# Kernel tuning notes

Measured on AMD Instinct MI355X. Metric: run time of the kernel, lower is better.

## Reference

```python
import jax, jax.numpy as jnp
import numpy as np

L = 3          # encoder layers
H, D = 12, 64  # heads, head_dim
DM = H * D     # 768
DF = 3072
WH = WW = 14
S = WH * WW + 1            # 197 tokens incl. cls
ND = (2*WH-1)*(2*WW-1) + 3  # 732 rel-pos entries
EPS = 1e-12


def _make_rel_idx():
    coords = np.stack(np.meshgrid(np.arange(WH), np.arange(WW), indexing='ij'))
    coords = coords.reshape(2, -1)                      # [2, 196]
    rel = (coords[:, :, None] - coords[:, None, :]).transpose(1, 2, 0)  # [196,196,2]
    rel[:, :, 0] += WH - 1
    rel[:, :, 1] += WW - 1
    rel[:, :, 0] *= 2 * WW - 1
    idx = np.zeros((S, S), dtype=np.int32)
    idx[1:, 1:] = rel.sum(-1)
    idx[0, :] = ND - 3
    idx[:, 0] = ND - 2
    idx[0, 0] = ND - 1
    return jnp.asarray(idx.flatten())

REL_IDX = _make_rel_idx()


def _ln(x, g, b):
    m = jnp.mean(x, -1, keepdims=True)
    v = jnp.mean(jnp.square(x - m), -1, keepdims=True)
    return (x - m) * jax.lax.rsqrt(v + EPS) * g + b


def setup_inputs() -> dict:
    key = jax.random.key(0)
    ks = iter(jax.random.split(key, 32))
    p = lambda *s: jax.random.normal(next(ks), s, jnp.float32) * 0.02
    inp = {
        'x': jax.random.normal(next(ks), (64, WH, WW, DM), jnp.float32),
        'cls': p(1, 1, DM),
        'g1': jnp.ones((L, DM)), 'b1': jnp.zeros((L, DM)),
        'Wq': p(L, DM, DM), 'bq': jnp.zeros((L, DM)),
        'Wk': p(L, DM, DM),
        'Wv': p(L, DM, DM), 'bv': jnp.zeros((L, DM)),
        'rel_tbl': p(L, ND, H),
        'Wo': p(L, DM, DM), 'bo': jnp.zeros((L, DM)),
        'lam1': jnp.full((L, DM), 0.1),
        'g2': jnp.ones((L, DM)), 'b2': jnp.zeros((L, DM)),
        'Wi': p(L, DM, DF), 'bi': jnp.zeros((L, DF)),
        'Wmo': p(L, DF, DM), 'bmo': jnp.zeros((L, DM)),
        'lam2': jnp.full((L, DM), 0.1),
    }
    return inp


def reference(x, cls, g1, b1, Wq, bq, Wk, Wv, bv, rel_tbl, Wo, bo, lam1,
              g2, b2, Wi, bi, Wmo, bmo, lam2):
    B = x.shape[0]
    # patchemb: NHWC -> NCHW -> [B, C, HW] -> [B, HW, C], prepend cls token
    t = jnp.transpose(x, (0, 3, 1, 2)).reshape(B, DM, WH * WW)
    t = jnp.transpose(t, (0, 2, 1))
    h = jnp.concatenate([jnp.broadcast_to(cls, (B, 1, DM)), t], axis=1)  # [B,S,DM]

    scale = 1.0 / np.sqrt(D)
    for i in range(L):
        r = h
        hn = _ln(h, g1[i], b1[i])
        q = (hn @ Wq[i] + bq[i]).reshape(B, S, H, D)
        k = (hn @ Wk[i]).reshape(B, S, H, D)
        v = (hn @ Wv[i] + bv[i]).reshape(B, S, H, D)
        scores = jnp.einsum('bqhd,bkhd->bhqk', q, k) * scale   # [B,H,S,S]
        rel = rel_tbl[i][REL_IDX].reshape(S, S, H)             # gather bias table
        scores = scores + jnp.transpose(rel, (2, 0, 1))[None]
        probs = jax.nn.softmax(scores, axis=-1)
        ctx = jnp.einsum('bhqk,bkhd->bqhd', probs, v).reshape(B, S, DM)
        h = r + (ctx @ Wo[i] + bo[i]) * lam1[i]
        r = h
        hn = _ln(h, g2[i], b2[i])
        ff = jax.nn.gelu(hn @ Wi[i] + bi[i], approximate=False) @ Wmo[i] + bmo[i]
        h = r + ff * lam2[i]
    return h  # final encoder output [B, S, DM]
```

## Files before the change

kernel.cpp:

```cpp
#include <hip/hip_runtime.h>

#define DMM 768
#define DFF 3072
#define NH  12
#define HD  64
#define SQ  197
#define BA  64
#define NDD 732
#define MROWS (BA*SQ)
#define MPAD  12672
#define PCOLS 224
#define KS2   72
#define VTS   232
#define QS    2304
#define BIASN (NH*208*208)

typedef unsigned short u16;
typedef __bf16 bf16x8 __attribute__((ext_vector_type(8)));
typedef float  f32x4  __attribute__((ext_vector_type(4)));
typedef unsigned short us8 __attribute__((ext_vector_type(8)));

__device__ __forceinline__ u16 f2b(float f) {
    unsigned v; __builtin_memcpy(&v, &f, 4);
    unsigned r = v + 0x7FFFu + ((v >> 16) & 1u);
    return (u16)(r >> 16);
}
__device__ __forceinline__ float gelu_exact(float x) {
    return 0.5f * x * (1.0f + erff(x * 0.70710678118654752f));
}
__device__ __forceinline__ void gload16(const u16* g, u16* l) {
    __builtin_amdgcn_global_load_lds(
        (const __attribute__((address_space(1))) unsigned int*)(g),
        (__attribute__((address_space(3))) unsigned int*)(l), 16, 0, 0);
}
__device__ __forceinline__ void hard_barrier() {
    asm volatile("s_waitcnt lgkmcnt(0)" ::: "memory");
    __builtin_amdgcn_s_barrier();
}

__global__ __launch_bounds__(256) void patchln_k(
    const float* __restrict__ x, const float* __restrict__ cls,
    const float* __restrict__ g, const float* __restrict__ b,
    float* __restrict__ h, u16* __restrict__ hn) {
    int row = blockIdx.x, tid = threadIdx.x;
    float x0 = 0.0f, x1 = 0.0f, x2 = 0.0f;
    if (row < MROWS) {
        int bb = row / SQ, s = row % SQ;
        const float* src = (s == 0) ? cls : &x[((long)bb * 196 + (s - 1)) * DMM];
        x0 = src[tid]; x1 = src[tid + 256]; x2 = src[tid + 512];
    }
    float* hr = h + (long)row * DMM;
    hr[tid] = x0; hr[tid + 256] = x1; hr[tid + 512] = x2;
    float s = x0 + x1 + x2, sq = x0 * x0 + x1 * x1 + x2 * x2;
    #pragma unroll
    for (int m = 32; m > 0; m >>= 1) {
        s  += __shfl_xor(s,  m, 64);
        sq += __shfl_xor(sq, m, 64);
    }
    __shared__ float ls[4], lq[4];
    int w = tid >> 6;
    if ((tid & 63) == 0) { ls[w] = s; lq[w] = sq; }
    __syncthreads();
    s  = ls[0] + ls[1] + ls[2] + ls[3];
    sq = lq[0] + lq[1] + lq[2] + lq[3];
    float mean = s * (1.0f / DMM);
    float var  = fmaxf(sq * (1.0f / DMM) - mean * mean, 0.0f);
    float rs = rsqrtf(var + 1e-12f);
    u16* hnr = hn + (long)row * DMM;
    hnr[tid]       = f2b((x0 - mean) * rs * g[tid]       + b[tid]);
    hnr[tid + 256] = f2b((x1 - mean) * rs * g[tid + 256] + b[tid + 256]);
    hnr[tid + 512] = f2b((x2 - mean) * rs * g[tid + 512] + b[tid + 512]);
}

__global__ __launch_bounds__(256) void tcast_k(const float* __restrict__ in,
                                               u16* __restrict__ out,
                                               int Kd, int Nd) {
    __shared__ float t[32][33];
    int k0 = blockIdx.x * 32, n0 = blockIdx.y * 32;
    int tx = threadIdx.x & 31, ty = threadIdx.x >> 5;
    #pragma unroll
    for (int i = 0; i < 4; ++i)
        t[tx][ty + 8 * i] = in[(long)(k0 + ty + 8 * i) * Nd + n0 + tx];
    __syncthreads();
    #pragma unroll
    for (int i = 0; i < 4; ++i)
        out[(long)(n0 + ty + 8 * i) * Kd + k0 + tx] = f2b(t[ty + 8 * i][tx]);
}

__global__ __launch_bounds__(256) void tcast4_k(
    const float* __restrict__ s0, const float* __restrict__ s1,
    const float* __restrict__ s2, const float* __restrict__ s3,
    u16* __restrict__ d0, u16* __restrict__ d1,
    u16* __restrict__ d2, u16* __restrict__ d3) {
    __shared__ float t[32][33];
    int z = blockIdx.z;
    const float* in = (z == 0) ? s0 : (z == 1) ? s1 : (z == 2) ? s2 : s3;
    u16* out = (z == 0) ? d0 : (z == 1) ? d1 : (z == 2) ? d2 : d3;
    int k0 = blockIdx.x * 32, n0 = blockIdx.y * 32;
    int tx = threadIdx.x & 31, ty = threadIdx.x >> 5;
    #pragma unroll
    for (int i = 0; i < 4; ++i)
        t[tx][ty + 8 * i] = in[(long)(k0 + ty + 8 * i) * DMM + n0 + tx];
    __syncthreads();
    #pragma unroll
    for (int i = 0; i < 4; ++i)
        out[(long)(n0 + ty + 8 * i) * DMM + k0 + tx] = f2b(t[ty + 8 * i][tx]);
}

__global__ __launch_bounds__(256) void ln_k(const float* __restrict__ h,
                                            const float* __restrict__ g,
                                            const float* __restrict__ b,
                                            u16* __restrict__ hn) {
    int row = blockIdx.x, tid = threadIdx.x;
    const float* hr = h + (long)row * DMM;
    float x0 = hr[tid], x1 = hr[tid + 256], x2 = hr[tid + 512];
    float s = x0 + x1 + x2, sq = x0 * x0 + x1 * x1 + x2 * x2;
    #pragma unroll
    for (int m = 32; m > 0; m >>= 1) {
        s  += __shfl_xor(s,  m, 64);
        sq += __shfl_xor(sq, m, 64);
    }
    __shared__ float ls[4], lq[4];
    int w = tid >> 6;
    if ((tid & 63) == 0) { ls[w] = s; lq[w] = sq; }
    __syncthreads();
    s  = ls[0] + ls[1] + ls[2] + ls[3];
    sq = lq[0] + lq[1] + lq[2] + lq[3];
    float mean = s * (1.0f / DMM);
    float var  = fmaxf(sq * (1.0f / DMM) - mean * mean, 0.0f);
    float rs = rsqrtf(var + 1e-12f);
    u16* hnr = hn + (long)row * DMM;
    hnr[tid]       = f2b((x0 - mean) * rs * g[tid]       + b[tid]);
    hnr[tid + 256] = f2b((x1 - mean) * rs * g[tid + 256] + b[tid + 256]);
    hnr[tid + 512] = f2b((x2 - mean) * rs * g[tid + 512] + b[tid + 512]);
}

template <int EPI>
__global__ __launch_bounds__(256) void gemm_bt(
    const u16* __restrict__ A, const u16* __restrict__ BT,
    const float* __restrict__ bias, u16* __restrict__ outB,
    float* __restrict__ hio, const float* __restrict__ lam,
    float* __restrict__ hout, int K, int N) {
    __shared__ __align__(16) u16 pool[16384];
    int tid = threadIdx.x;
    int w = tid >> 6, lane = tid & 63;
    int wr = w >> 1, wc = w & 1;
    int m16 = lane & 15;
    int kq  = (lane >> 4) * 8;
    int kq4 = (lane >> 4) * 4;

    int nwg = gridDim.x, bid = blockIdx.x;
    int qd = nwg >> 3, rm = nwg & 7;
    int xcd = bid & 7, seq = bid >> 3;
    int wg = (xcd < rm ? xcd * (qd + 1) : rm * (qd + 1) + (xcd - rm) * qd) + seq;
    int ntn = N >> 7;
    long m0 = (long)(wg / ntn) * 128;
    long n0 = (long)(wg % ntn) * 128;

    f32x4 acc[4][4] = {};

    int row_a = tid >> 2;
    int col_a = (tid & 3) * 8;
    const u16* gA0 = &A[(m0 + row_a) * (long)K + col_a];
    const u16* gA1 = &A[(m0 + 64 + row_a) * (long)K + col_a];
    const u16* gB0 = &BT[(n0 + row_a) * (long)K + col_a];
    const u16* gB1 = &BT[(n0 + 64 + row_a) * (long)K + col_a];
    int wo = w * 512;

    u16* const b0 = pool;
    u16* const b1 = pool + 8192;

    auto stage = [&](int k, u16* buf) {
        int k0 = k << 5;
        gload16(gA0 + k0, buf + wo);
        gload16(gA1 + k0, buf + 2048 + wo);
        gload16(gB0 + k0, buf + 4096 + wo);
        gload16(gB1 + k0, buf + 6144 + wo);
    };
    auto compute = [&](const u16* buf) {
        bf16x8 af[4], bf[4];
        #pragma unroll
        for (int i = 0; i < 4; ++i)
            af[i] = *(const bf16x8*)&buf[(wr * 64 + i * 16 + m16) * 32 + kq];
        #pragma unroll
        for (int j = 0; j < 4; ++j)
            bf[j] = *(const bf16x8*)&buf[4096 + (wc * 64 + j * 16 + m16) * 32 + kq];
        #pragma unroll
        for (int i = 0; i < 4; ++i)
            #pragma unroll
            for (int j = 0; j < 4; ++j)
                acc[i][j] = __builtin_amdgcn_mfma_f32_16x16x32_bf16(
                    af[i], bf[j], acc[i][j], 0, 0, 0);
    };

    const int nsteps = K >> 5;
    stage(0, b0);
    for (int ks = 0; ks < nsteps - 2; ks += 2) {
        stage(ks + 1, b1);
        asm volatile("s_waitcnt vmcnt(4)" ::: "memory");
        __builtin_amdgcn_s_barrier();
        compute(b0);
        hard_barrier();
        stage(ks + 2, b0);
        asm volatile("s_waitcnt vmcnt(4)" ::: "memory");
        __builtin_amdgcn_s_barrier();
        compute(b1);
        hard_barrier();
    }
    stage(nsteps - 1, b1);
    asm volatile("s_waitcnt vmcnt(4)" ::: "memory");
    __builtin_amdgcn_s_barrier();
    compute(b0);
    hard_barrier();
    asm volatile("s_waitcnt vmcnt(0)" ::: "memory");
    __builtin_amdgcn_s_barrier();
    compute(b1);

    hard_barrier();
    float* Cs = (float*)pool;
    float bcol[4];
    #pragma unroll
    for (int j = 0; j < 4; ++j)
        bcol[j] = bias ? bias[n0 + wc * 64 + j * 16 + m16] : 0.0f;
    int et4 = tid * 4;
    int colr = et4 & 127;
    f32x4 lam4 = {};
    if (EPI == 2) lam4 = *(const f32x4*)&lam[n0 + colr];

    #pragma unroll
    for (int p = 0; p < 2; ++p) {
        if (p) hard_barrier();
        if (wr == p) {
            #pragma unroll
            for (int i = 0; i < 4; ++i)
                #pragma unroll
                for (int j = 0; j < 4; ++j)
                    #pragma unroll
                    for (int r = 0; r < 4; ++r)
                        Cs[(i * 16 + kq4 + r) * 128 + wc * 64 + j * 16 + m16] =
                            acc[i][j][r] + bcol[j];
        }
        hard_barrier();
        #pragma unroll
        for (int k = 0; k < 8; ++k) {
            int e0 = k * 1024 + et4;
            int row = e0 >> 7;
            f32x4 v = *(const f32x4*)&Cs[row * 128 + colr];
            long grow = m0 + p * 64 + row;
            long gi = grow * (long)N + n0 + colr;
            if (EPI == 0) {
                uint2 o;
                o.x = (unsigned)f2b(v[0]) | ((unsigned)f2b(v[1]) << 16);
                o.y = (unsigned)f2b(v[2]) | ((unsigned)f2b(v[3]) << 16);
                *(uint2*)&outB[gi] = o;
            } else if (EPI == 1) {
                uint2 o;
                o.x = (unsigned)f2b(gelu_exact(v[0])) | ((unsigned)f2b(gelu_exact(v[1])) << 16);
                o.y = (unsigned)f2b(gelu_exact(v[2])) | ((unsigned)f2b(gelu_exact(v[3])) << 16);
                *(uint2*)&outB[gi] = o;
            } else {
                f32x4 hv = *(f32x4*)&hio[gi];
                #pragma unroll
                for (int t = 0; t < 4; ++t) hv[t] += v[t] * lam4[t];
                *(f32x4*)&hio[gi] = hv;
                if (hout != nullptr && grow < MROWS)
                    *(f32x4*)&hout[gi] = hv;
            }
        }
    }
}

__device__ __forceinline__ int relidx(int q, int k) {
    if (q == 0 && k == 0) return NDD - 1;
    if (k == 0) return NDD - 2;
    if (q == 0) return NDD - 3;
    int a = q - 1, c = k - 1;
    int dh = a / 14 - c / 14 + 13;
    int dw = a % 14 - c % 14 + 13;
    return dh * 27 + dw;
}

__global__ void bias_k(const float* __restrict__ rel, float* __restrict__ bias,
                       const float* __restrict__ bq, const float* __restrict__ bv,
                       float* __restrict__ bqkv) {
    int idx = blockIdx.x * 256 + threadIdx.x;
    if (idx < BIASN) {
        int hh = idx / (208 * 208);
        int r = (idx / 208) % 208, c = idx % 208;
        float v = 0.0f;
        if (r < SQ && c < SQ) v = rel[relidx(r, c) * NH + hh];
        bias[idx] = v;
    } else {
        int i = idx - BIASN;
        if (i < QS)
            bqkv[i] = (i < 768) ? bq[i] : ((i < 1536) ? 0.0f : bv[i - 1536]);
    }
}

__global__ __launch_bounds__(256) void attn_qk(
    const u16* __restrict__ QKV, const float* __restrict__ bias,
    u16* __restrict__ P) {
    int bh = blockIdx.x;
    int b = bh / NH, hh = bh % NH;
    __shared__ u16 Ks[208 * KS2];
    int tid = threadIdx.x, w = tid >> 6, lane = tid & 63;
    long base = ((long)b * SQ) * QS + hh * HD;
    const u16* Qp = QKV;
    const u16* Kp = QKV + 768;
    u16* Pb = P + (long)bh * 208 * PCOLS;
    for (int idx = tid; idx < 208 * 16; idx += 256)
        Pb[(idx >> 4) * PCOLS + 208 + (idx & 15)] = 0;
    for (int idx = tid; idx < 208 * 8; idx += 256) {
        int row = idx >> 3, dg = (idx & 7) * 8;
        us8 kv = {};
        if (row < SQ) kv = *(const us8*)&Kp[base + (long)row * QS + dg];
        *(us8*)&Ks[row * KS2 + dg] = kv;
    }
    __syncthreads();
    int m16 = lane & 15, quad = lane >> 4;
    int kq8 = quad * 8, q4 = quad * 4;
    const float* bh_bias = bias + (long)hh * 208 * 208;
    for (int t = w; t < 13; t += 4) {
        int m0 = t * 16;
        int qrow = m0 + m16; if (qrow > SQ - 1) qrow = SQ - 1;
        bf16x8 a0 = *(const bf16x8*)&Qp[base + (long)qrow * QS + kq8];
        bf16x8 a1 = *(const bf16x8*)&Qp[base + (long)qrow * QS + 32 + kq8];
        f32x4 sc[13];
        #pragma unroll
        for (int n = 0; n < 13; ++n) {
            bf16x8 b0 = *(const bf16x8*)&Ks[(n * 16 + m16) * KS2 + kq8];
            bf16x8 b1 = *(const bf16x8*)&Ks[(n * 16 + m16) * KS2 + 32 + kq8];
            f32x4 z = {};
            z = __builtin_amdgcn_mfma_f32_16x16x32_bf16(a0, b0, z, 0, 0, 0);
            z = __builtin_amdgcn_mfma_f32_16x16x32_bf16(a1, b1, z, 0, 0, 0);
            sc[n] = z;
        }
        float mx[4] = {-3e38f, -3e38f, -3e38f, -3e38f};
        #pragma unroll
        for (int n = 0; n < 13; ++n) {
            int col = n * 16 + m16;
            bool valid = col < SQ;
            #pragma unroll
            for (int r = 0; r < 4; ++r) {
                float v = sc[n][r] * 0.125f + bh_bias[(m0 + q4 + r) * 208 + col];
                v = valid ? v : -3e38f;
                sc[n][r] = v;
                mx[r] = fmaxf(mx[r], v);
            }
        }
        #pragma unroll
        for (int r = 0; r < 4; ++r)
            #pragma unroll
            for (int msk = 1; msk < 16; msk <<= 1)
                mx[r] = fmaxf(mx[r], __shfl_xor(mx[r], msk, 64));
        float sum[4] = {0, 0, 0, 0};
        #pragma unroll
        for (int n = 0; n < 13; ++n)
            #pragma unroll
            for (int r = 0; r < 4; ++r) {
                float e = __expf(sc[n][r] - mx[r]);
                sc[n][r] = e;
                sum[r] += e;
            }
        #pragma unroll
        for (int r = 0; r < 4; ++r)
            #pragma unroll
            for (int msk = 1; msk < 16; msk <<= 1)
                sum[r] += __shfl_xor(sum[r], msk, 64);
        float inv[4];
        #pragma unroll
        for (int r = 0; r < 4; ++r) inv[r] = 1.0f / sum[r];
        #pragma unroll
        for (int n = 0; n < 13; ++n) {
            int col = n * 16 + m16;
            #pragma unroll
            for (int r = 0; r < 4; ++r)
                Pb[(m0 + q4 + r) * PCOLS + col] = f2b(sc[n][r] * inv[r]);
        }
    }
}

__global__ __launch_bounds__(256) void attn_pv(
    const u16* __restrict__ P, const u16* __restrict__ QKV,
    u16* __restrict__ ctx) {
    int bh = blockIdx.x;
    int b = bh / NH, hh = bh % NH;
    __shared__ u16 Vt[64 * VTS];
    int tid = threadIdx.x, w = tid >> 6, lane = tid & 63;
    long base  = ((long)b * SQ) * QS + 1536 + hh * HD;
    long basec = ((long)b * SQ) * DMM + hh * HD;
    const u16* Vp = QKV;
    for (int idx = tid; idx < 224 * 8; idx += 256) {
        int row = idx >> 3, dg = (idx & 7) * 8;
        us8 vv = {};
        if (row < SQ) vv = *(const us8*)&Vp[base + (long)row * QS + dg];
        #pragma unroll
        for (int j = 0; j < 8; ++j) Vt[(dg + j) * VTS + row] = vv[j];
    }
    __syncthreads();
    const u16* Pb = P + (long)bh * 208 * PCOLS;
    int m16 = lane & 15, quad = lane >> 4;
    int kq8 = quad * 8, q4 = quad * 4;
    for (int t = w; t < 13; t += 4) {
        int m0 = t * 16;
        f32x4 co[4] = {};
        #pragma unroll
        for (int ks = 0; ks < 7; ++ks) {
            bf16x8 ap = *(const bf16x8*)&Pb[(m0 + m16) * PCOLS + ks * 32 + kq8];
            #pragma unroll
            for (int n = 0; n < 4; ++n) {
                bf16x8 bv = *(const bf16x8*)&Vt[(n * 16 + m16) * VTS + ks * 32 + kq8];
                co[n] = __builtin_amdgcn_mfma_f32_16x16x32_bf16(ap, bv, co[n], 0, 0, 0);
            }
        }
        #pragma unroll
        for (int n = 0; n < 4; ++n) {
            int col = n * 16 + m16;
            #pragma unroll
            for (int r = 0; r < 4; ++r) {
                int qr = m0 + q4 + r;
                if (qr < SQ) ctx[basec + (long)qr * DMM + col] = f2b(co[n][r]);
            }
        }
    }
}

extern "C" void kernel_launch(void* const* d_in, const int* in_sizes, int n_in,
                              void* d_out, int out_size, void* d_ws, size_t ws_size,
                              hipStream_t stream) {
    const float* x    = (const float*)d_in[0];
    const float* cls  = (const float*)d_in[1];
    const float* g1   = (const float*)d_in[2];
    const float* b1   = (const float*)d_in[3];
    const float* Wq   = (const float*)d_in[4];
    const float* bq   = (const float*)d_in[5];
    const float* Wk   = (const float*)d_in[6];
    const float* Wv   = (const float*)d_in[7];
    const float* bv   = (const float*)d_in[8];
    const float* rel  = (const float*)d_in[9];
    const float* Wo   = (const float*)d_in[10];
    const float* bo   = (const float*)d_in[11];
    const float* lam1 = (const float*)d_in[12];
    const float* g2   = (const float*)d_in[13];
    const float* b2   = (const float*)d_in[14];
    const float* Wi   = (const float*)d_in[15];
    const float* bi   = (const float*)d_in[16];
    const float* Wmo  = (const float*)d_in[17];
    const float* bmo  = (const float*)d_in[18];
    const float* lam2 = (const float*)d_in[19];

    char* p = (char*)d_ws;
    auto alloc = [&](size_t bytes) -> void* {
        void* r = (void*)p;
        p += (bytes + 255) & ~(size_t)255;
        return r;
    };
    float* h     = (float*)alloc((size_t)MPAD * DMM * 4);
    u16*   hn    = (u16*)alloc((size_t)MPAD * DMM * 2);
    u16*   qkvb  = (u16*)alloc((size_t)MPAD * QS * 2);
    u16*   ffh   = (u16*)alloc((size_t)MPAD * DFF * 2);
    u16*   WqkvT = (u16*)alloc((size_t)QS * DMM * 2);
    u16*   WoT   = (u16*)alloc((size_t)DMM * DMM * 2);
    u16*   WiT   = (u16*)alloc((size_t)DMM * DFF * 2);
    u16*   WmoT  = (u16*)alloc((size_t)DFF * DMM * 2);
    float* biasb = (float*)alloc((size_t)NH * 208 * 208 * 4);
    float* bqkv  = (float*)alloc((size_t)QS * 4);
    u16*   ctxb  = hn;
    u16*   Pbuf  = ffh;

    dim3 tg4(DMM / 32, DMM / 32, 4);
    dim3 tg2(DMM / 32, DFF / 32);
    dim3 tg3(DFF / 32, DMM / 32);
    int gqkv = (MPAD / 128) * (QS / 128);
    int g6   = (MPAD / 128) * (DMM / 128);
    int g24  = (MPAD / 128) * (DFF / 128);

    patchln_k<<<MPAD, 256, 0, stream>>>(x, cls, g1, b1, h, hn);

    for (int i = 0; i < 3; ++i) {
        size_t wofs  = (size_t)i * DMM * DMM;
        size_t wofs2 = (size_t)i * DMM * DFF;
        tcast4_k<<<tg4, 256, 0, stream>>>(Wq + wofs, Wk + wofs, Wv + wofs, Wo + wofs,
                                          WqkvT, WqkvT + 768 * DMM,
                                          WqkvT + 2 * 768 * DMM, WoT);
        tcast_k<<<tg2, 256, 0, stream>>>(Wi + wofs2, WiT, DMM, DFF);
        tcast_k<<<tg3, 256, 0, stream>>>(Wmo + wofs2, WmoT, DFF, DMM);
        bias_k<<<(BIASN + QS + 255) / 256, 256, 0, stream>>>(
            rel + (size_t)i * NDD * NH, biasb, bq + i * DMM, bv + i * DMM, bqkv);

        if (i > 0)
            ln_k<<<MPAD, 256, 0, stream>>>(h, g1 + i * DMM, b1 + i * DMM, hn);
        gemm_bt<0><<<gqkv, 256, 0, stream>>>(hn, WqkvT, bqkv, qkvb, nullptr, nullptr, nullptr, DMM, QS);
        attn_qk<<<BA * NH, 256, 0, stream>>>(qkvb, biasb, Pbuf);
        attn_pv<<<BA * NH, 256, 0, stream>>>(Pbuf, qkvb, ctxb);
        gemm_bt<2><<<g6, 256, 0, stream>>>(ctxb, WoT, bo + i * DMM, nullptr, h, lam1 + i * DMM, nullptr, DMM, DMM);
        ln_k<<<MPAD, 256, 0, stream>>>(h, g2 + i * DMM, b2 + i * DMM, hn);
        gemm_bt<1><<<g24, 256, 0, stream>>>(hn, WiT, bi + i * DFF, ffh, nullptr, nullptr, nullptr, DMM, DFF);
        gemm_bt<2><<<g6, 256, 0, stream>>>(ffh, WmoT, bmo + i * DMM, nullptr, h, lam2 + i * DMM,
                                           (i == 2) ? (float*)d_out : nullptr, DFF, DMM);
    }
}
```

Before: 1.330 ms.

## Fuse QK-softmax and PV attention kernels, keep probabilities in LDS

Merges the two attention kernels into one per (batch, head) block. The softmax probability tile now stays in shared memory instead of being written to and re-read from a global buffer, and the K staging area is reused for the transposed V tile. This removes the global-memory round trip of the P matrix and one kernel launch per layer. In exchange each block uses about 126 KB of dynamic LDS, which reduces how many blocks can be resident per CU.

```diff
diff --git a/kernel.cpp b/kernel.cpp
--- a/kernel.cpp
+++ b/kernel.cpp
@@ -9,8 +9,8 @@
 #define NDD 732
 #define MROWS (BA*SQ)
 #define MPAD  12672
-#define PCOLS 224
 #define KS2   72
+#define PPS   232
 #define VTS   232
 #define QS    2304
 #define BIASN (NH*208*208)
@@ -297,19 +297,20 @@
     }
 }
 
-__global__ __launch_bounds__(256) void attn_qk(
+__global__ __launch_bounds__(256) void attn_k(
     const u16* __restrict__ QKV, const float* __restrict__ bias,
-    u16* __restrict__ P) {
+    u16* __restrict__ ctx) {
+    extern __shared__ __align__(16) u16 apool[];
+    u16* Ks = apool;
+    u16* Ps = apool + 14976;
     int bh = blockIdx.x;
     int b = bh / NH, hh = bh % NH;
-    __shared__ u16 Ks[208 * KS2];
     int tid = threadIdx.x, w = tid >> 6, lane = tid & 63;
     long base = ((long)b * SQ) * QS + hh * HD;
     const u16* Qp = QKV;
     const u16* Kp = QKV + 768;
-    u16* Pb = P + (long)bh * 208 * PCOLS;
     for (int idx = tid; idx < 208 * 16; idx += 256)
-        Pb[(idx >> 4) * PCOLS + 208 + (idx & 15)] = 0;
+        Ps[(idx >> 4) * PPS + 208 + (idx & 15)] = 0;
     for (int idx = tid; idx < 208 * 8; idx += 256) {
         int row = idx >> 3, dg = (idx & 7) * 8;
         us8 kv = {};
@@ -375,38 +376,27 @@
             int col = n * 16 + m16;
             #pragma unroll
             for (int r = 0; r < 4; ++r)
-                Pb[(m0 + q4 + r) * PCOLS + col] = f2b(sc[n][r] * inv[r]);
-        }
-    }
-}
-
-__global__ __launch_bounds__(256) void attn_pv(
-    const u16* __restrict__ P, const u16* __restrict__ QKV,
-    u16* __restrict__ ctx) {
-    int bh = blockIdx.x;
-    int b = bh / NH, hh = bh % NH;
-    __shared__ u16 Vt[64 * VTS];
-    int tid = threadIdx.x, w = tid >> 6, lane = tid & 63;
-    long base  = ((long)b * SQ) * QS + 1536 + hh * HD;
-    long basec = ((long)b * SQ) * DMM + hh * HD;
-    const u16* Vp = QKV;
+                Ps[(m0 + q4 + r) * PPS + col] = f2b(sc[n][r] * inv[r]);
+        }
+    }
+    __syncthreads();
+    u16* Vt = Ks;
+    long vbase = base + 1536;
     for (int idx = tid; idx < 224 * 8; idx += 256) {
         int row = idx >> 3, dg = (idx & 7) * 8;
         us8 vv = {};
-        if (row < SQ) vv = *(const us8*)&Vp[base + (long)row * QS + dg];
+        if (row < SQ) vv = *(const us8*)&QKV[vbase + (long)row * QS + dg];
         #pragma unroll
         for (int j = 0; j < 8; ++j) Vt[(dg + j) * VTS + row] = vv[j];
     }
     __syncthreads();
-    const u16* Pb = P + (long)bh * 208 * PCOLS;
-    int m16 = lane & 15, quad = lane >> 4;
-    int kq8 = quad * 8, q4 = quad * 4;
+    long basec = ((long)b * SQ) * DMM + hh * HD;
     for (int t = w; t < 13; t += 4) {
         int m0 = t * 16;
         f32x4 co[4] = {};
         #pragma unroll
         for (int ks = 0; ks < 7; ++ks) {
-            bf16x8 ap = *(const bf16x8*)&Pb[(m0 + m16) * PCOLS + ks * 32 + kq8];
+            bf16x8 ap = *(const bf16x8*)&Ps[(m0 + m16) * PPS + ks * 32 + kq8];
             #pragma unroll
             for (int n = 0; n < 4; ++n) {
                 bf16x8 bv = *(const bf16x8*)&Vt[(n * 16 + m16) * VTS + ks * 32 + kq8];
@@ -466,7 +456,6 @@
     float* biasb = (float*)alloc((size_t)NH * 208 * 208 * 4);
     float* bqkv  = (float*)alloc((size_t)QS * 4);
     u16*   ctxb  = hn;
-    u16*   Pbuf  = ffh;
 
     dim3 tg4(DMM / 32, DMM / 32, 4);
     dim3 tg2(DMM / 32, DFF / 32);
@@ -474,6 +463,7 @@
     int gqkv = (MPAD / 128) * (QS / 128);
     int g6   = (MPAD / 128) * (DMM / 128);
     int g24  = (MPAD / 128) * (DFF / 128);
+    const size_t ALDS = (size_t)(208 * KS2 + 208 * PPS) * 2;
 
     patchln_k<<<MPAD, 256, 0, stream>>>(x, cls, g1, b1, h, hn);
 
@@ -491,8 +481,7 @@
         if (i > 0)
             ln_k<<<MPAD, 256, 0, stream>>>(h, g1 + i * DMM, b1 + i * DMM, hn);
         gemm_bt<0><<<gqkv, 256, 0, stream>>>(hn, WqkvT, bqkv, qkvb, nullptr, nullptr, nullptr, DMM, QS);
-        attn_qk<<<BA * NH, 256, 0, stream>>>(qkvb, biasb, Pbuf);
-        attn_pv<<<BA * NH, 256, 0, stream>>>(Pbuf, qkvb, ctxb);
+        attn_k<<<BA * NH, 256, ALDS, stream>>>(qkvb, biasb, ctxb);
         gemm_bt<2><<<g6, 256, 0, stream>>>(ctxb, WoT, bo + i * DMM, nullptr, h, lam1 + i * DMM, nullptr, DMM, DMM);
         ln_k<<<MPAD, 256, 0, stream>>>(h, g2 + i * DMM, b2 + i * DMM, hn);
         gemm_bt<1><<<g24, 256, 0, stream>>>(hn, WiT, bi + i * DFF, ffh, nullptr, nullptr, nullptr, DMM, DFF);
```

After: 1.377 ms. 3.5% more time.
